# Optimization experiments

Hardware: AMD Instinct MI355X
Metric: run time of the kernel (lower is better)

The kernel has to match this reference:

```python
import jax, jax.numpy as jnp
import numpy as np

B, L, H, E = 4, 2048, 8, 64
S, D = L, E  # causal mask forces L == S


def setup_inputs() -> dict:
    key = jax.random.key(0)
    kq, kk, kv, km = jax.random.split(key, 4)
    return {
        "queries": jax.random.normal(kq, (B, L, H, E), dtype=jnp.float32),
        "keys": jax.random.normal(kk, (B, S, H, E), dtype=jnp.float32),
        "values": jax.random.normal(kv, (B, S, H, D), dtype=jnp.float32),
        "map": jax.random.normal(km, (S, S), dtype=jnp.float32),
    }


def reference(queries, keys, values, map):
    # queries: [B,L,H,E], keys: [B,S,H,E], values: [B,S,H,D], map: [S,S]
    E_ = queries.shape[-1]
    scale = 1.0 / jnp.sqrt(jnp.asarray(E_, dtype=queries.dtype))
    # raw attention scores: [B,H,L,S]
    scores = jnp.einsum("blhe,bshe->bhls", queries, keys)
    # mix scores with learned map along the key axis: [B,H,L,S]
    scores = jnp.einsum("bhls,st->bhlt", scores, map)
    # causal mask (TriangularCausalMask: triu with diagonal=1 is masked)
    Lq = queries.shape[1]
    causal = jnp.triu(jnp.ones((Lq, Lq), dtype=bool), k=1)  # [L,S]
    scores = jnp.where(causal[None, None, :, :], -jnp.inf, scores)
    attn = jax.nn.softmax(scale * scores, axis=-1)  # dropout p=0.0 -> identity
    out = jnp.einsum("bhls,bshd->blhd", attn, values)  # [B,L,H,D]
    return out
```

## Files before the change

kernel.cpp:

```cpp
#include <hip/hip_runtime.h>


typedef short bf16x8 __attribute__((ext_vector_type(8)));
typedef float f32x4 __attribute__((ext_vector_type(4)));
typedef float f32x16 __attribute__((ext_vector_type(16)));
typedef unsigned short u16x8 __attribute__((ext_vector_type(8)));
typedef unsigned int u32x4 __attribute__((ext_vector_type(4)));

typedef __attribute__((address_space(1))) const void gvoid;
typedef __attribute__((address_space(3))) void lvoid;

__device__ __forceinline__ unsigned short f2bf(float x) {
  unsigned int u = __float_as_uint(x);
  u += 0x7FFFu + ((u >> 16) & 1u);
  return (unsigned short)(u >> 16);
}
__device__ __forceinline__ float bf2f(unsigned short h) {
  return __uint_as_float(((unsigned int)h) << 16);
}
__device__ __forceinline__ unsigned int cvtpk(float lo, float hi) {
  unsigned int r;
  asm("v_cvt_pk_bf16_f32 %0, %1, %2" : "=v"(r) : "v"(lo), "v"(hi));
  return r;
}

__device__ __forceinline__ void gload16(const unsigned short* g, unsigned short* l) {
  __builtin_amdgcn_global_load_lds((gvoid*)g, (lvoid*)l, 16, 0, 0);
}

template <int NW>
__device__ __forceinline__ void stage_tile(const unsigned short* __restrict__ g,
                                           int gstride, unsigned short* l,
                                           int rows, int tid) {
  const int lane = tid & 63, w = tid >> 6;
  const int nch = rows << 3;
  for (int c0 = (w << 6); c0 < nch; c0 += NW * 64) {
    const int c = c0 + lane;
    const int row = c >> 3;
    const int bir = (c & 7) << 4;
    const int sb = bir ^ ((row & 7) << 4);
    gload16(g + (size_t)row * gstride + (sb >> 1), l + (size_t)c0 * 8);
  }
}

__device__ __forceinline__ int swz(int row, int byteInRow) {
  return row * 128 + (byteInRow ^ ((row & 7) << 4));
}

__device__ __forceinline__ int chunk_off(int c, int gstride) {
  return (c >> 3) * gstride + ((((c & 7) ^ ((c >> 3) & 7))) << 3);
}

__global__ __launch_bounds__(256) void prep_m(const float* __restrict__ M,
                                              unsigned short* __restrict__ Mh,
                                              unsigned short* __restrict__ Ml) {
  __shared__ float Ts[64][68];
  const int s0 = blockIdx.x << 6, t0 = blockIdx.y << 6;
  const int tid = threadIdx.x, r = tid >> 2, c0 = (tid & 3) << 4;
  const float* src = M + (size_t)(s0 + r) * 2048 + t0 + c0;
#pragma unroll
  for (int j = 0; j < 4; ++j)
    *(float4*)&Ts[r][c0 + 4 * j] = *(const float4*)(src + 4 * j);
  __syncthreads();
  u16x8 h0, h1, l0v, l1v;
#pragma unroll
  for (int j = 0; j < 8; ++j) {
    float x = Ts[c0 + j][r];
    unsigned short hh = f2bf(x);
    h0[j] = hh; l0v[j] = f2bf(x - bf2f(hh));
  }
#pragma unroll
  for (int j = 8; j < 16; ++j) {
    float x = Ts[c0 + j][r];
    unsigned short hh = f2bf(x);
    h1[j - 8] = hh; l1v[j - 8] = f2bf(x - bf2f(hh));
  }
  const size_t o = (size_t)(t0 + r) * 2048 + s0 + c0;
  *(u16x8*)(Mh + o) = h0; *(u16x8*)(Mh + o + 8) = h1;
  *(u16x8*)(Ml + o) = l0v; *(u16x8*)(Ml + o + 8) = l1v;
}

__global__ __launch_bounds__(256) void prep_kv(const float* __restrict__ src4d,
                                               unsigned short* __restrict__ Dh,
                                               unsigned short* __restrict__ Dl,
                                               int has_lo) {
  __shared__ float Ts[64][68];
  const int s0 = blockIdx.x << 6, bh = blockIdx.y;
  const int b = bh >> 3, h = bh & 7;
  const int tid = threadIdx.x, r = tid >> 2, c0 = (tid & 3) << 4;
  const float* src = src4d + ((size_t)(b * 2048 + s0 + r) * 8 + h) * 64 + c0;
#pragma unroll
  for (int j = 0; j < 4; ++j)
    *(float4*)&Ts[r][c0 + 4 * j] = *(const float4*)(src + 4 * j);
  __syncthreads();
  u16x8 h0, h1, l0v, l1v;
#pragma unroll
  for (int j = 0; j < 8; ++j) {
    float x = Ts[c0 + j][r];
    unsigned short hh = f2bf(x);
    h0[j] = hh; l0v[j] = f2bf(x - bf2f(hh));
  }
#pragma unroll
  for (int j = 8; j < 16; ++j) {
    float x = Ts[c0 + j][r];
    unsigned short hh = f2bf(x);
    h1[j - 8] = hh; l1v[j - 8] = f2bf(x - bf2f(hh));
  }
  const size_t o = ((size_t)bh * 64 + r) * 2048 + s0 + c0;
  *(u16x8*)(Dh + o) = h0; *(u16x8*)(Dh + o + 8) = h1;
  if (has_lo) { *(u16x8*)(Dl + o) = l0v; *(u16x8*)(Dl + o + 8) = l1v; }
}

__global__ __launch_bounds__(256) void km_mfma(
    const unsigned short* __restrict__ Mth, const unsigned short* __restrict__ Mtl,
    const unsigned short* __restrict__ Kth, const unsigned short* __restrict__ Ktl,
    unsigned short* __restrict__ KMh, unsigned short* __restrict__ KMl) {
  __shared__ __attribute__((aligned(16))) unsigned short sm[24576];
  unsigned short* MtH = sm;
  unsigned short* MtL = sm + 8192;
  unsigned short* KtH = sm + 16384;
  unsigned short* KtL = sm + 20480;
  const int tid = threadIdx.x, lane = tid & 63, w = tid >> 6;
  const int g = lane >> 4, li = lane & 15;
  const int t0 = blockIdx.x << 7;
  const int bh = blockIdx.y;
  const unsigned short* KtHb = Kth + (size_t)bh * 64 * 2048;
  const unsigned short* KtLb = Ktl + (size_t)bh * 64 * 2048;

  f32x4 acc[2][4];
#pragma unroll
  for (int mi = 0; mi < 2; ++mi)
#pragma unroll
    for (int ni = 0; ni < 4; ++ni) acc[mi][ni] = (f32x4){0.f, 0.f, 0.f, 0.f};

  for (int s0 = 0; s0 < 2048; s0 += 64) {
    __syncthreads();
    stage_tile<4>(Mth + (size_t)t0 * 2048 + s0, 2048, MtH, 128, tid);
    stage_tile<4>(Mtl + (size_t)t0 * 2048 + s0, 2048, MtL, 128, tid);
    stage_tile<4>(KtHb + s0, 2048, KtH, 64, tid);
    stage_tile<4>(KtLb + s0, 2048, KtL, 64, tid);
    asm volatile("s_waitcnt vmcnt(0)" ::: "memory");
    __syncthreads();
#pragma unroll
    for (int kk = 0; kk < 2; ++kk) {
      const int kb = (kk * 32 + 8 * g) * 2;
      bf16x8 aH[2], aL[2];
#pragma unroll
      for (int mi = 0; mi < 2; ++mi) {
        const int row = (w << 5) + (mi << 4) + li;
        aH[mi] = *(const bf16x8*)((const char*)MtH + swz(row, kb));
        aL[mi] = *(const bf16x8*)((const char*)MtL + swz(row, kb));
      }
#pragma unroll
      for (int ni = 0; ni < 4; ++ni) {
        const int row = (ni << 4) + li;
        const int off = swz(row, kb);
        const bf16x8 bH = *(const bf16x8*)((const char*)KtH + off);
        const bf16x8 bL = *(const bf16x8*)((const char*)KtL + off);
#pragma unroll
        for (int mi = 0; mi < 2; ++mi) {
          acc[mi][ni] = __builtin_amdgcn_mfma_f32_16x16x32_bf16(aH[mi], bH, acc[mi][ni], 0, 0, 0);
          acc[mi][ni] = __builtin_amdgcn_mfma_f32_16x16x32_bf16(aH[mi], bL, acc[mi][ni], 0, 0, 0);
          acc[mi][ni] = __builtin_amdgcn_mfma_f32_16x16x32_bf16(aL[mi], bH, acc[mi][ni], 0, 0, 0);
        }
      }
    }
  }
  const size_t base = (size_t)bh * 2048 * 64;
#pragma unroll
  for (int mi = 0; mi < 2; ++mi)
#pragma unroll
    for (int r = 0; r < 4; ++r) {
      const int trow = t0 + (w << 5) + (mi << 4) + (g << 2) + r;
#pragma unroll
      for (int ni = 0; ni < 4; ++ni) {
        const float x = acc[mi][ni][r];
        const unsigned short hh = f2bf(x);
        const size_t idx = base + (size_t)trow * 64 + (ni << 4) + li;
        KMh[idx] = hh;
        KMl[idx] = f2bf(x - bf2f(hh));
      }
    }
}

__global__ __launch_bounds__(256, 4) void attn32(
    const float* __restrict__ Q, const unsigned short* __restrict__ KMh,
    const unsigned short* __restrict__ KMl, const unsigned short* __restrict__ Vt,
    unsigned short* __restrict__ Opart, float* __restrict__ Ml) {
  __shared__ __attribute__((aligned(16))) unsigned short sm[20480];
  const int tid = threadIdx.x, lane = tid & 63, w = tid >> 6;
  const int g2 = lane >> 5, li5 = lane & 31;

  const int bid = (int)blockIdx.x;
  const int x = bid & 7, n = bid >> 3;
  const int slot = n >> 5, j = n & 31;
  const int bh = (x << 2) | (j & 3);
  const int k = j >> 2;
  const int hf = slot & 1;
  const int lt = (slot < 2) ? (15 - k) : k;
  const int half = lt + 1;
  const int jt0 = hf * half;
  const int jtEnd = jt0 + half - 1;
  const int b = bh >> 3, h = bh & 7;
  const int l0 = lt << 7;
  const int qg = l0 + (w << 5) + li5;
  const int rloc = (w << 5) + li5;

  const int c0 = tid, c1 = tid + 256;
  const int ko0 = chunk_off(c0, 64), ko1 = chunk_off(c1, 64);
  const int vo0 = chunk_off(c0, 2048), vo1 = chunk_off(c1, 2048);
  const int ld0 = c0 << 3, ld1 = c1 << 3;
  unsigned short* VTl = sm + 16384;

  const float SC2 = 0.18033688011112042f;
  bf16x8 qh[4], ql[4];
  {
    const float* qsrc = Q + (((size_t)(b * 2048 + qg) * 8 + h) << 6) + (g2 << 3);
#pragma unroll
    for (int kki = 0; kki < 4; ++kki) {
      const float4 v0 = *(const float4*)(qsrc + 16 * kki);
      const float4 v1 = *(const float4*)(qsrc + 16 * kki + 4);
      const float xs[8] = {v0.x, v0.y, v0.z, v0.w, v1.x, v1.y, v1.z, v1.w};
#pragma unroll
      for (int jj = 0; jj < 8; ++jj) {
        const float xv = xs[jj] * SC2;
        const unsigned short hh = f2bf(xv);
        qh[kki][jj] = (short)hh;
        ql[kki][jj] = (short)f2bf(xv - bf2f(hh));
      }
    }
  }

  f32x16 o0 = {0,0,0,0,0,0,0,0,0,0,0,0,0,0,0,0};
  f32x16 o1 = {0,0,0,0,0,0,0,0,0,0,0,0,0,0,0,0};
  f32x16 lsacc = {0,0,0,0,0,0,0,0,0,0,0,0,0,0,0,0};
  float m2 = -1e30f;
  bf16x8 ones;
#pragma unroll
  for (int jj = 0; jj < 8; ++jj) ones[jj] = (short)0x3F80;

  const unsigned short* khsrc = KMh + (size_t)bh * 2048 * 64 + (size_t)jt0 * 4096;
  const unsigned short* klsrc = KMl + (size_t)bh * 2048 * 64 + (size_t)jt0 * 4096;
  const unsigned short* vsrc = Vt + (size_t)bh * 64 * 2048 + jt0 * 64;

  const int jtmax_w = 2 * lt + (w >> 1);

  {
    unsigned short* kb = sm + ((jt0 & 1) << 13);
    gload16(khsrc + ko0, kb + ld0);
    gload16(khsrc + ko1, kb + ld1);
    gload16(klsrc + ko0, kb + 4096 + ld0);
    gload16(klsrc + ko1, kb + 4096 + ld1);
  }
  khsrc += 4096; klsrc += 4096;
  asm volatile("s_waitcnt vmcnt(0)" ::: "memory");
  __builtin_amdgcn_s_barrier();
  __builtin_amdgcn_sched_barrier(0);

  for (int jt = jt0; jt <= jtEnd; ++jt) {
    gload16(vsrc + vo0, VTl + ld0);
    gload16(vsrc + vo1, VTl + ld1);
    {
      unsigned short* kb = sm + (((jt + 1) & 1) << 13);
      gload16(khsrc + ko0, kb + ld0);
      gload16(khsrc + ko1, kb + ld1);
      gload16(klsrc + ko0, kb + 4096 + ld0);
      gload16(klsrc + ko1, kb + 4096 + ld1);
    }
    khsrc += 4096; klsrc += 4096; vsrc += 64;

    const bool act = (jt <= jtmax_w);
    bf16x8 pf[4];
    if (act) {
      const unsigned short* KH = sm + ((jt & 1) << 13);
      const unsigned short* KL = KH + 4096;

      f32x16 z0 = {0,0,0,0,0,0,0,0,0,0,0,0,0,0,0,0};
      f32x16 z1 = {0,0,0,0,0,0,0,0,0,0,0,0,0,0,0,0};
      __builtin_amdgcn_s_setprio(1);
#pragma unroll
      for (int kki = 0; kki < 4; ++kki) {
        const int cb = 32 * kki + 16 * g2;
        const bf16x8 a0h = *(const bf16x8*)((const char*)KH + swz(li5, cb));
        const bf16x8 a0l = *(const bf16x8*)((const char*)KL + swz(li5, cb));
        const bf16x8 a1h = *(const bf16x8*)((const char*)KH + swz(32 + li5, cb));
        const bf16x8 a1l = *(const bf16x8*)((const char*)KL + swz(32 + li5, cb));
        z0 = __builtin_amdgcn_mfma_f32_32x32x16_bf16(a0h, qh[kki], z0, 0, 0, 0);
        z0 = __builtin_amdgcn_mfma_f32_32x32x16_bf16(a0h, ql[kki], z0, 0, 0, 0);
        z0 = __builtin_amdgcn_mfma_f32_32x32x16_bf16(a0l, qh[kki], z0, 0, 0, 0);
        z1 = __builtin_amdgcn_mfma_f32_32x32x16_bf16(a1h, qh[kki], z1, 0, 0, 0);
        z1 = __builtin_amdgcn_mfma_f32_32x32x16_bf16(a1h, ql[kki], z1, 0, 0, 0);
        z1 = __builtin_amdgcn_mfma_f32_32x32x16_bf16(a1l, qh[kki], z1, 0, 0, 0);
      }
      __builtin_amdgcn_s_setprio(0);

      const bool needmask = (jt * 64 + 63 > l0 + (w << 5));
      if (needmask) {
        const int thr = qg - jt * 64;
#pragma unroll
        for (int rr = 0; rr < 16; ++rr) {
          const int tl = (g2 << 2) + ((rr >> 2) << 3) + (rr & 3);
          if (tl > thr) z0[rr] = -1e30f;
          if (tl + 32 > thr) z1[rr] = -1e30f;
        }
      }

      float t16[16];
#pragma unroll
      for (int rr = 0; rr < 16; ++rr) t16[rr] = fmaxf(z0[rr], z1[rr]);
#pragma unroll
      for (int s = 8; s; s >>= 1)
#pragma unroll
        for (int rr = 0; rr < 8; ++rr)
          if (rr < s) t16[rr] = fmaxf(t16[rr], t16[rr + s]);
      const float mx = fmaxf(t16[0], __shfl_xor(t16[0], 32));
      if (__any(mx > m2 + 11.0f)) {
        const float m2n = fmaxf(m2, mx);
        const float fs = exp2f(m2 - m2n);
        m2 = m2n;
#pragma unroll
        for (int rr = 0; rr < 16; ++rr) { o0[rr] *= fs; o1[rr] *= fs; }
        lsacc[0] *= fs;
      }

      float pv0[16], pv1[16];
#pragma unroll
      for (int rr = 0; rr < 16; ++rr) {
        pv0[rr] = exp2f(z0[rr] - m2);
        pv1[rr] = exp2f(z1[rr] - m2);
      }
      unsigned int W0[8], W1[8];
#pragma unroll
      for (int i = 0; i < 8; ++i) {
        W0[i] = cvtpk(pv0[2 * i], pv0[2 * i + 1]);
        W1[i] = cvtpk(pv1[2 * i], pv1[2 * i + 1]);
      }
      asm volatile("v_permlane32_swap_b32 %0, %1" : "+v"(W0[0]), "+v"(W0[2]));
      asm volatile("v_permlane32_swap_b32 %0, %1" : "+v"(W0[1]), "+v"(W0[3]));
      asm volatile("v_permlane32_swap_b32 %0, %1" : "+v"(W0[4]), "+v"(W0[6]));
      asm volatile("v_permlane32_swap_b32 %0, %1" : "+v"(W0[5]), "+v"(W0[7]));
      asm volatile("v_permlane32_swap_b32 %0, %1" : "+v"(W1[0]), "+v"(W1[2]));
      asm volatile("v_permlane32_swap_b32 %0, %1" : "+v"(W1[1]), "+v"(W1[3]));
      asm volatile("v_permlane32_swap_b32 %0, %1" : "+v"(W1[4]), "+v"(W1[6]));
      asm volatile("v_permlane32_swap_b32 %0, %1" : "+v"(W1[5]), "+v"(W1[7]));
      {
        u32x4 f0 = {W0[0], W0[1], W0[2], W0[3]};
        u32x4 f1 = {W0[4], W0[5], W0[6], W0[7]};
        u32x4 f2 = {W1[0], W1[1], W1[2], W1[3]};
        u32x4 f3 = {W1[4], W1[5], W1[6], W1[7]};
        pf[0] = __builtin_bit_cast(bf16x8, f0);
        pf[1] = __builtin_bit_cast(bf16x8, f1);
        pf[2] = __builtin_bit_cast(bf16x8, f2);
        pf[3] = __builtin_bit_cast(bf16x8, f3);
      }
    }

    asm volatile("s_waitcnt vmcnt(4)" ::: "memory");
    __builtin_amdgcn_s_barrier();
    __builtin_amdgcn_sched_barrier(0);

    if (act) {
      __builtin_amdgcn_s_setprio(1);
#pragma unroll
      for (int kki = 0; kki < 4; ++kki) {
        const int cb = 32 * kki + 16 * g2;
        const bf16x8 v0f = *(const bf16x8*)((const char*)VTl + swz(li5, cb));
        const bf16x8 v1f = *(const bf16x8*)((const char*)VTl + swz(32 + li5, cb));
        o0 = __builtin_amdgcn_mfma_f32_32x32x16_bf16(v0f, pf[kki], o0, 0, 0, 0);
        o1 = __builtin_amdgcn_mfma_f32_32x32x16_bf16(v1f, pf[kki], o1, 0, 0, 0);
        lsacc = __builtin_amdgcn_mfma_f32_32x32x16_bf16(ones, pf[kki], lsacc, 0, 0, 0);
      }
      __builtin_amdgcn_s_setprio(0);
    }

    asm volatile("s_waitcnt vmcnt(0)" ::: "memory");
    __builtin_amdgcn_s_barrier();
    __builtin_amdgcn_sched_barrier(0);
  }

  const size_t pidx = (((size_t)bh * 16 + lt) << 7) + rloc;
  unsigned short* op = Opart + (size_t)hf * 4194304 + pidx * 64;
#pragma unroll
  for (int r2 = 0; r2 < 4; ++r2) {
    const int doff = (g2 << 2) + (r2 << 3);
    uint2 pa, pb;
    pa.x = cvtpk(o0[4 * r2], o0[4 * r2 + 1]);
    pa.y = cvtpk(o0[4 * r2 + 2], o0[4 * r2 + 3]);
    *(uint2*)(op + doff) = pa;
    pb.x = cvtpk(o1[4 * r2], o1[4 * r2 + 1]);
    pb.y = cvtpk(o1[4 * r2 + 2], o1[4 * r2 + 3]);
    *(uint2*)(op + 32 + doff) = pb;
  }
  float* mlp = Ml + (((size_t)hf * 65536) + pidx) * 2;
  mlp[0] = m2;
  mlp[1] = lsacc[0];
}

__global__ __launch_bounds__(256) void attn_combine(
    const unsigned short* __restrict__ Opart, const float* __restrict__ Ml,
    float* __restrict__ Out) {
  const int tid = threadIdx.x;
  const int rowg = (int)blockIdx.x * 32 + (tid >> 3);
  const int d0 = (tid & 7) << 3;
  const int r = rowg & 127;
  const int lt = (rowg >> 7) & 15;
  const int bh = rowg >> 11;
  const int b = bh >> 3, h = bh & 7;
  const size_t pidx = (((size_t)bh * 16 + lt) << 7) + r;
  const size_t HOFF = 4194304;
  const size_t MOFF = 131072;
  const float m0 = Ml[pidx * 2], ls0 = Ml[pidx * 2 + 1];
  const float m1 = Ml[MOFF + pidx * 2], ls1 = Ml[MOFF + pidx * 2 + 1];
  const float mm = fmaxf(m0, m1);
  const float w0 = exp2f(m0 - mm), w1 = exp2f(m1 - mm);
  const float inv = 1.f / (ls0 * w0 + ls1 * w1);
  const u16x8 A = *(const u16x8*)(Opart + pidx * 64 + d0);
  const u16x8 Bv = *(const u16x8*)(Opart + HOFF + pidx * 64 + d0);
  float res[8];
#pragma unroll
  for (int jj = 0; jj < 8; ++jj)
    res[jj] = (bf2f(A[jj]) * w0 + bf2f(Bv[jj]) * w1) * inv;
  const int qg = (lt << 7) + r;
  float* o = Out + (((size_t)(b * 2048 + qg) * 8 + h) << 6) + d0;
  *(float4*)o = make_float4(res[0], res[1], res[2], res[3]);
  *(float4*)(o + 4) = make_float4(res[4], res[5], res[6], res[7]);
}

extern "C" void kernel_launch(void* const* d_in, const int* in_sizes, int n_in,
                              void* d_out, int out_size, void* d_ws, size_t ws_size,
                              hipStream_t stream) {
  const float* Q = (const float*)d_in[0];
  const float* K = (const float*)d_in[1];
  const float* V = (const float*)d_in[2];
  const float* M = (const float*)d_in[3];
  float* Out = (float*)d_out;
  char* ws = (char*)d_ws;
  const size_t MB = 1u << 20;
  unsigned short* Mth = (unsigned short*)(ws);
  unsigned short* Mtl = (unsigned short*)(ws + 8 * MB);
  unsigned short* Kth = (unsigned short*)(ws + 16 * MB);
  unsigned short* Ktl = (unsigned short*)(ws + 24 * MB);
  unsigned short* Vts = (unsigned short*)(ws + 32 * MB);
  unsigned short* KMh = (unsigned short*)(ws + 40 * MB);
  unsigned short* KMl = (unsigned short*)(ws + 48 * MB);
  unsigned short* Opart = (unsigned short*)(ws);
  float* Mlp = (float*)(ws + 16 * MB);

  prep_m<<<dim3(32, 32), 256, 0, stream>>>(M, Mth, Mtl);
  prep_kv<<<dim3(32, 32), 256, 0, stream>>>(K, Kth, Ktl, 1);
  prep_kv<<<dim3(32, 32), 256, 0, stream>>>(V, Vts, (unsigned short*)nullptr, 0);
  km_mfma<<<dim3(16, 32), 256, 0, stream>>>(Mth, Mtl, Kth, Ktl, KMh, KMl);
  attn32<<<dim3(1024), 256, 0, stream>>>(Q, KMh, KMl, Vts, Opart, Mlp);
  attn_combine<<<dim3(2048), 256, 0, stream>>>(Opart, Mlp, Out);
}
```

Before: 169.2 us.

## Use 256-row query tiles with 512-thread blocks and double-buffered K/V staging

The attention kernel now uses 512-thread blocks that each cover 256 query rows instead of 128, halving the grid to 512 blocks. Each staged K/V tile is therefore reused by twice as many rows. V is now double-buffered together with K through stage_tile, which removes the mid-iteration barrier that waited for V. The change costs more shared memory per block and fewer, larger blocks, which may reduce occupancy and make causal load balance coarser.

```diff
diff --git a/kernel.cpp b/kernel.cpp
--- a/kernel.cpp
+++ b/kernel.cpp
@@ -45,10 +45,6 @@
 
 __device__ __forceinline__ int swz(int row, int byteInRow) {
   return row * 128 + (byteInRow ^ ((row & 7) << 4));
-}
-
-__device__ __forceinline__ int chunk_off(int c, int gstride) {
-  return (c >> 3) * gstride + ((((c & 7) ^ ((c >> 3) & 7))) << 3);
 }
 
 __global__ __launch_bounds__(256) void prep_m(const float* __restrict__ M,
@@ -183,11 +179,11 @@
     }
 }
 
-__global__ __launch_bounds__(256, 4) void attn32(
+__global__ __launch_bounds__(512, 4) void attn32(
     const float* __restrict__ Q, const unsigned short* __restrict__ KMh,
     const unsigned short* __restrict__ KMl, const unsigned short* __restrict__ Vt,
     unsigned short* __restrict__ Opart, float* __restrict__ Ml) {
-  __shared__ __attribute__((aligned(16))) unsigned short sm[20480];
+  __shared__ __attribute__((aligned(16))) unsigned short sm[24576];
   const int tid = threadIdx.x, lane = tid & 63, w = tid >> 6;
   const int g2 = lane >> 5, li5 = lane & 31;
 
@@ -196,21 +192,15 @@
   const int slot = n >> 5, j = n & 31;
   const int bh = (x << 2) | (j & 3);
   const int k = j >> 2;
-  const int hf = slot & 1;
-  const int lt = (slot < 2) ? (15 - k) : k;
-  const int half = lt + 1;
+  const int hf = slot;
+  const int lt = slot ? k : (7 - k);
+  const int half = 2 * lt + 2;
   const int jt0 = hf * half;
   const int jtEnd = jt0 + half - 1;
   const int b = bh >> 3, h = bh & 7;
-  const int l0 = lt << 7;
+  const int l0 = lt << 8;
   const int qg = l0 + (w << 5) + li5;
   const int rloc = (w << 5) + li5;
-
-  const int c0 = tid, c1 = tid + 256;
-  const int ko0 = chunk_off(c0, 64), ko1 = chunk_off(c1, 64);
-  const int vo0 = chunk_off(c0, 2048), vo1 = chunk_off(c1, 2048);
-  const int ld0 = c0 << 3, ld1 = c1 << 3;
-  unsigned short* VTl = sm + 16384;
 
   const float SC2 = 0.18033688011112042f;
   bf16x8 qh[4], ql[4];
@@ -239,41 +229,35 @@
 #pragma unroll
   for (int jj = 0; jj < 8; ++jj) ones[jj] = (short)0x3F80;
 
-  const unsigned short* khsrc = KMh + (size_t)bh * 2048 * 64 + (size_t)jt0 * 4096;
-  const unsigned short* klsrc = KMl + (size_t)bh * 2048 * 64 + (size_t)jt0 * 4096;
-  const unsigned short* vsrc = Vt + (size_t)bh * 64 * 2048 + jt0 * 64;
-
-  const int jtmax_w = 2 * lt + (w >> 1);
+  const unsigned short* KHb = KMh + (size_t)bh * 2048 * 64;
+  const unsigned short* KLb = KMl + (size_t)bh * 2048 * 64;
+  const unsigned short* VTb = Vt + (size_t)bh * 64 * 2048;
+
+  const int jtmax_w = (lt << 2) + (w >> 1);
 
   {
-    unsigned short* kb = sm + ((jt0 & 1) << 13);
-    gload16(khsrc + ko0, kb + ld0);
-    gload16(khsrc + ko1, kb + ld1);
-    gload16(klsrc + ko0, kb + 4096 + ld0);
-    gload16(klsrc + ko1, kb + 4096 + ld1);
-  }
-  khsrc += 4096; klsrc += 4096;
+    unsigned short* s0b = sm + (jt0 & 1) * 12288;
+    stage_tile<8>(KHb + (size_t)jt0 * 4096, 64, s0b, 64, tid);
+    stage_tile<8>(KLb + (size_t)jt0 * 4096, 64, s0b + 4096, 64, tid);
+    stage_tile<8>(VTb + jt0 * 64, 2048, s0b + 8192, 64, tid);
+  }
   asm volatile("s_waitcnt vmcnt(0)" ::: "memory");
   __builtin_amdgcn_s_barrier();
   __builtin_amdgcn_sched_barrier(0);
 
   for (int jt = jt0; jt <= jtEnd; ++jt) {
-    gload16(vsrc + vo0, VTl + ld0);
-    gload16(vsrc + vo1, VTl + ld1);
-    {
-      unsigned short* kb = sm + (((jt + 1) & 1) << 13);
-      gload16(khsrc + ko0, kb + ld0);
-      gload16(khsrc + ko1, kb + ld1);
-      gload16(klsrc + ko0, kb + 4096 + ld0);
-      gload16(klsrc + ko1, kb + 4096 + ld1);
+    const int cur = jt & 1;
+    if (jt < jtEnd) {
+      unsigned short* nb = sm + (cur ^ 1) * 12288;
+      stage_tile<8>(KHb + (size_t)(jt + 1) * 4096, 64, nb, 64, tid);
+      stage_tile<8>(KLb + (size_t)(jt + 1) * 4096, 64, nb + 4096, 64, tid);
+      stage_tile<8>(VTb + (jt + 1) * 64, 2048, nb + 8192, 64, tid);
     }
-    khsrc += 4096; klsrc += 4096; vsrc += 64;
-
-    const bool act = (jt <= jtmax_w);
-    bf16x8 pf[4];
-    if (act) {
-      const unsigned short* KH = sm + ((jt & 1) << 13);
+
+    if (jt <= jtmax_w) {
+      const unsigned short* KH = sm + cur * 12288;
       const unsigned short* KL = KH + 4096;
+      const unsigned short* VT = KH + 8192;
 
       f32x16 z0 = {0,0,0,0,0,0,0,0,0,0,0,0,0,0,0,0};
       f32x16 z1 = {0,0,0,0,0,0,0,0,0,0,0,0,0,0,0,0};
@@ -343,6 +327,7 @@
       asm volatile("v_permlane32_swap_b32 %0, %1" : "+v"(W1[1]), "+v"(W1[3]));
       asm volatile("v_permlane32_swap_b32 %0, %1" : "+v"(W1[4]), "+v"(W1[6]));
       asm volatile("v_permlane32_swap_b32 %0, %1" : "+v"(W1[5]), "+v"(W1[7]));
+      bf16x8 pf[4];
       {
         u32x4 f0 = {W0[0], W0[1], W0[2], W0[3]};
         u32x4 f1 = {W0[4], W0[5], W0[6], W0[7]};
@@ -353,19 +338,13 @@
         pf[2] = __builtin_bit_cast(bf16x8, f2);
         pf[3] = __builtin_bit_cast(bf16x8, f3);
       }
-    }
-
-    asm volatile("s_waitcnt vmcnt(4)" ::: "memory");
-    __builtin_amdgcn_s_barrier();
-    __builtin_amdgcn_sched_barrier(0);
-
-    if (act) {
+
       __builtin_amdgcn_s_setprio(1);
 #pragma unroll
       for (int kki = 0; kki < 4; ++kki) {
         const int cb = 32 * kki + 16 * g2;
-        const bf16x8 v0f = *(const bf16x8*)((const char*)VTl + swz(li5, cb));
-        const bf16x8 v1f = *(const bf16x8*)((const char*)VTl + swz(32 + li5, cb));
+        const bf16x8 v0f = *(const bf16x8*)((const char*)VT + swz(li5, cb));
+        const bf16x8 v1f = *(const bf16x8*)((const char*)VT + swz(32 + li5, cb));
         o0 = __builtin_amdgcn_mfma_f32_32x32x16_bf16(v0f, pf[kki], o0, 0, 0, 0);
         o1 = __builtin_amdgcn_mfma_f32_32x32x16_bf16(v1f, pf[kki], o1, 0, 0, 0);
         lsacc = __builtin_amdgcn_mfma_f32_32x32x16_bf16(ones, pf[kki], lsacc, 0, 0, 0);
@@ -378,7 +357,7 @@
     __builtin_amdgcn_sched_barrier(0);
   }
 
-  const size_t pidx = (((size_t)bh * 16 + lt) << 7) + rloc;
+  const size_t pidx = (((size_t)bh * 8 + lt) << 8) + rloc;
   unsigned short* op = Opart + (size_t)hf * 4194304 + pidx * 64;
 #pragma unroll
   for (int r2 = 0; r2 < 4; ++r2) {
@@ -402,11 +381,11 @@
   const int tid = threadIdx.x;
   const int rowg = (int)blockIdx.x * 32 + (tid >> 3);
   const int d0 = (tid & 7) << 3;
-  const int r = rowg & 127;
-  const int lt = (rowg >> 7) & 15;
+  const int r = rowg & 255;
+  const int lt = (rowg >> 8) & 7;
   const int bh = rowg >> 11;
   const int b = bh >> 3, h = bh & 7;
-  const size_t pidx = (((size_t)bh * 16 + lt) << 7) + r;
+  const size_t pidx = (((size_t)bh * 8 + lt) << 8) + r;
   const size_t HOFF = 4194304;
   const size_t MOFF = 131072;
   const float m0 = Ml[pidx * 2], ls0 = Ml[pidx * 2 + 1];
@@ -420,7 +399,7 @@
 #pragma unroll
   for (int jj = 0; jj < 8; ++jj)
     res[jj] = (bf2f(A[jj]) * w0 + bf2f(Bv[jj]) * w1) * inv;
-  const int qg = (lt << 7) + r;
+  const int qg = (lt << 8) + r;
   float* o = Out + (((size_t)(b * 2048 + qg) * 8 + h) << 6) + d0;
   *(float4*)o = make_float4(res[0], res[1], res[2], res[3]);
   *(float4*)(o + 4) = make_float4(res[4], res[5], res[6], res[7]);
@@ -450,6 +429,6 @@
   prep_kv<<<dim3(32, 32), 256, 0, stream>>>(K, Kth, Ktl, 1);
   prep_kv<<<dim3(32, 32), 256, 0, stream>>>(V, Vts, (unsigned short*)nullptr, 0);
   km_mfma<<<dim3(16, 32), 256, 0, stream>>>(Mth, Mtl, Kth, Ktl, KMh, KMl);
-  attn32<<<dim3(1024), 256, 0, stream>>>(Q, KMh, KMl, Vts, Opart, Mlp);
+  attn32<<<dim3(512), 512, 0, stream>>>(Q, KMh, KMl, Vts, Opart, Mlp);
   attn_combine<<<dim3(2048), 256, 0, stream>>>(Opart, Mlp, Out);
 }
```

New measurement: 169.8 us. Within noise of the previous version (+0.4%).
